# Optimization experiments

Hardware: AMD Instinct MI355X
Metric: run time of the kernel (lower is better)

Reference implementation:

```python
import jax, jax.numpy as jnp
import numpy as np

P = 16          # num_points (knots per piecewise-linear function)
LO, HI = -1.0, 1.0  # uniform knot grid range
EPS = 1e-6


def apl(x, v):
    """Adaptive piecewise-linear layer on a uniform grid.
    x: (N, I), v: (I, P, O) learnable knot values. out[n,o] = sum_i interp_i(x[n,i])."""
    I, Pk, O = v.shape
    t = (jnp.clip(x, LO, HI) - LO) / (HI - LO) * (Pk - 1)   # (N, I) in [0, P-1]
    idx = jnp.clip(jnp.floor(t), 0, Pk - 2).astype(jnp.int32)
    frac = t - idx
    ar = jnp.arange(Pk)
    # sparse interpolation weights (N, I, P): two nonzeros per (n, i)
    w = (jnp.where(ar == idx[..., None], (1.0 - frac)[..., None], 0.0)
         + jnp.where(ar == idx[..., None] + 1, frac[..., None], 0.0))
    return jnp.einsum('nip,ipo->no', w, v)


def max_abs_normalize(h):
    B, T, D = h.shape
    hn = h.reshape(B * T, D)
    hn = hn / (jnp.max(jnp.abs(hn), axis=1, keepdims=True) + EPS)
    return hn.reshape(B, T, D)


def mingru_layer(x, h0, vz, vh):
    """x: (B,T,Din), h0: (B,D). Returns normalized hidden states (B,T,D)."""
    B, T, _ = x.shape
    xf = x.reshape(B * T, -1)
    h_bar = apl(xf, vh).reshape(B, T, -1)
    z = jax.nn.sigmoid(apl(xf, vz)).reshape(B, T, -1)
    a = 1.0 - z
    b = z * h_bar
    # unstable closed-form recurrence: h[t] = A[t] * (h0 + cumsum(b/A))
    A = jnp.cumprod(a, axis=1)
    S = jnp.cumsum(b / A, axis=1)
    h = A * (h0[:, None, :] + S)
    return max_abs_normalize(h)


def setup_inputs() -> dict:
    key = jax.random.key(0)
    ks = jax.random.split(key, 8)
    B, T, Din, D, Dout = 8, 2048, 64, 64, 64
    Z_OFF = -6.0 / Din  # bias z-layer output to ~-6 so sigmoid(z) is small -> cumprod stays finite
    x = jax.random.normal(ks[0], (B, T, Din), dtype=jnp.float32)
    def vz(k, I, O):
        return 0.05 * jax.random.normal(k, (I, P, O), dtype=jnp.float32) + Z_OFF
    def vh(k, I, O):
        return 0.5 * jax.random.normal(k, (I, P, O), dtype=jnp.float32)
    return {
        'x': x,
        'vz0': vz(ks[1], Din, D), 'vh0': vh(ks[2], Din, D),
        'vz1': vz(ks[3], D, D),   'vh1': vh(ks[4], D, D),
        'vz2': vz(ks[5], D, D),   'vh2': vh(ks[6], D, D),
        'vout': 0.5 * jax.random.normal(ks[7], (D, P, Dout), dtype=jnp.float32),
    }


def reference(x, vz0, vh0, vz1, vh1, vz2, vh2, vout):
    B, T, _ = x.shape
    D = vh0.shape[-1]
    h0 = jnp.zeros((B, D), dtype=x.dtype)
    cur = mingru_layer(x, h0, vz0, vh0)
    cur = mingru_layer(cur, h0, vz1, vh1)
    cur = mingru_layer(cur, h0, vz2, vh2)
    out = apl(cur.reshape(B * T, -1), vout).reshape(B, T, -1)
    return out
```

## Files before the change

kernel.cpp:

```cpp
#include <hip/hip_runtime.h>


#define WPB 4
#define NC 64
#define CL 32

__global__ __launch_bounds__(256) void prep_dual_kernel(
    const float* __restrict__ vz, const float* __restrict__ vh,
    float4* __restrict__ tab)
{
    int idx = blockIdx.x * blockDim.x + threadIdx.x;
    if (idx >= 64 * 15 * 64) return;
    int o = idx & 63;
    int p = (idx >> 6) % 15;
    int i = idx / (15 * 64);
    int base = (i * 16 + p) * 64 + o;
    float z0 = vz[base], z1 = vz[base + 64];
    float h0 = vh[base], h1 = vh[base + 64];
    tab[idx] = make_float4(z0, z1 - z0, h0, h1 - h0);
}

__global__ __launch_bounds__(256) void prep_out_kernel(
    const float* __restrict__ v, float2* __restrict__ tab)
{
    int idx = blockIdx.x * blockDim.x + threadIdx.x;
    if (idx >= 64 * 15 * 64) return;
    int o = idx & 63;
    int p = (idx >> 6) % 15;
    int i = idx / (15 * 64);
    int base = (i * 16 + p) * 64 + o;
    float v0 = v[base], v1 = v[base + 64];
    tab[idx] = make_float2(v0, v1 - v0);
}

__global__ __launch_bounds__(256) void apl_dual_kernel(
    const float* __restrict__ in, const float4* __restrict__ tab,
    float2* __restrict__ zh, int N)
{
    int lane = threadIdx.x & 63;
    int n = blockIdx.x * WPB + (threadIdx.x >> 6);
    if (n >= N) return;

    float xv = in[(size_t)n * 64 + lane];
    float accz = 0.f, acch = 0.f;
#pragma unroll
    for (int i = 0; i < 64; ++i) {
        float xi = __shfl(xv, i, 64);
        float t = (fminf(fmaxf(xi, -1.f), 1.f) + 1.f) * 7.5f;
        int idx = (int)t;
        idx = idx > 14 ? 14 : idx;
        float fr = t - (float)idx;
        float4 e = tab[(size_t)(i * 15 + idx) * 64 + lane];
        accz += fmaf(fr, e.y, e.x);
        acch += fmaf(fr, e.w, e.z);
    }
    float z = 1.f / (1.f + expf(-accz));
    zh[(size_t)n * 64 + lane] = make_float2(z, acch);
}

__global__ __launch_bounds__(256) void apl_out_kernel(
    const float* __restrict__ in, const float2* __restrict__ tab,
    float* __restrict__ out, int N)
{
    int lane = threadIdx.x & 63;
    int n = blockIdx.x * WPB + (threadIdx.x >> 6);
    if (n >= N) return;

    float xv = in[(size_t)n * 64 + lane];
    float acc = 0.f;
#pragma unroll
    for (int i = 0; i < 64; ++i) {
        float xi = __shfl(xv, i, 64);
        float t = (fminf(fmaxf(xi, -1.f), 1.f) + 1.f) * 7.5f;
        int idx = (int)t;
        idx = idx > 14 ? 14 : idx;
        float fr = t - (float)idx;
        float2 e = tab[(size_t)(i * 15 + idx) * 64 + lane];
        acc += fmaf(fr, e.y, e.x);
    }
    out[(size_t)n * 64 + lane] = acc;
}

__global__ __launch_bounds__(256) void scan_pass1_kernel(
    const float2* __restrict__ zh, float2* __restrict__ chunkAB, int T)
{
    int lane = threadIdx.x & 63;
    int wid = blockIdx.x * (blockDim.x >> 6) + (threadIdx.x >> 6);
    int b = wid / NC, c = wid % NC;
    const float2* p = zh + ((size_t)b * T + (size_t)c * CL) * 64 + lane;

    float A = 1.f, Bc = 0.f;
    for (int k0 = 0; k0 < CL; k0 += 8) {
        float2 v[8];
#pragma unroll
        for (int k = 0; k < 8; ++k) v[k] = p[(size_t)(k0 + k) * 64];
#pragma unroll
        for (int k = 0; k < 8; ++k) {
            float a = 1.f - v[k].x;
            float bb = v[k].x * v[k].y;
            A *= a;
            Bc = fmaf(a, Bc, bb);
        }
    }
    chunkAB[(size_t)wid * 64 + lane] = make_float2(A, Bc);
}

__global__ __launch_bounds__(64) void scan_fixup_kernel(
    const float2* __restrict__ chunkAB, float* __restrict__ hinit)
{
    int b = blockIdx.x;
    int d = threadIdx.x;
    const float2* p = chunkAB + (size_t)b * NC * 64 + d;
    float* o = hinit + (size_t)b * NC * 64 + d;

    float h = 0.f;
    for (int c0 = 0; c0 < NC; c0 += 8) {
        float2 ab[8];
#pragma unroll
        for (int k = 0; k < 8; ++k) ab[k] = p[(size_t)(c0 + k) * 64];
#pragma unroll
        for (int k = 0; k < 8; ++k) {
            o[(size_t)(c0 + k) * 64] = h;
            h = fmaf(ab[k].x, h, ab[k].y);
        }
    }
}

__global__ __launch_bounds__(256) void scan_pass2_kernel(
    const float2* __restrict__ zh, const float* __restrict__ hinit,
    float* __restrict__ out, int T)
{
    int lane = threadIdx.x & 63;
    int wid = blockIdx.x * (blockDim.x >> 6) + (threadIdx.x >> 6);
    int b = wid / NC, c = wid % NC;
    const float2* p = zh + ((size_t)b * T + (size_t)c * CL) * 64 + lane;
    float* o = out + ((size_t)b * T + (size_t)c * CL) * 64 + lane;

    float h = hinit[(size_t)wid * 64 + lane];
    for (int k0 = 0; k0 < CL; k0 += 8) {
        float2 v[8];
        float hs[8];
#pragma unroll
        for (int k = 0; k < 8; ++k) v[k] = p[(size_t)(k0 + k) * 64];
#pragma unroll
        for (int k = 0; k < 8; ++k) {
            h = fmaf(v[k].x, v[k].y - h, h);
            hs[k] = h;
        }
#pragma unroll
        for (int k = 0; k < 8; ++k) {
            float m = fabsf(hs[k]);
            m = fmaxf(m, __shfl_xor(m, 32, 64));
            m = fmaxf(m, __shfl_xor(m, 16, 64));
            m = fmaxf(m, __shfl_xor(m, 8, 64));
            m = fmaxf(m, __shfl_xor(m, 4, 64));
            m = fmaxf(m, __shfl_xor(m, 2, 64));
            m = fmaxf(m, __shfl_xor(m, 1, 64));
            o[(size_t)(k0 + k) * 64] = hs[k] / (m + 1e-6f);
        }
    }
}

extern "C" void kernel_launch(void* const* d_in, const int* in_sizes, int n_in,
                              void* d_out, int out_size, void* d_ws, size_t ws_size,
                              hipStream_t stream) {
    const float* x    = (const float*)d_in[0];
    const float* vz0  = (const float*)d_in[1];
    const float* vh0  = (const float*)d_in[2];
    const float* vz1  = (const float*)d_in[3];
    const float* vh1  = (const float*)d_in[4];
    const float* vz2  = (const float*)d_in[5];
    const float* vh2  = (const float*)d_in[6];
    const float* vout = (const float*)d_in[7];

    const int N = in_sizes[0] / 64;
    const int T = NC * CL;
    const int B = N / T;

    char* ws = (char*)d_ws;
    const size_t TAB_ELEMS = (size_t)64 * 15 * 64;
    float2* zh      = (float2*)ws;
    float*  cur     = (float*)(ws + 8388608);
    float4* tab0    = (float4*)(ws + 12582912);
    float4* tab1    = (float4*)(ws + 13565952);
    float4* tab2    = (float4*)(ws + 14548992);
    float2* tab_out = (float2*)(ws + 15532032);
    float2* chunkAB = (float2*)(ws + 16023552);
    float*  hinit   = (float*)(ws + 16285696);

    dim3 pblk(256), pgrd((TAB_ELEMS + 255) / 256);
    prep_dual_kernel<<<pgrd, pblk, 0, stream>>>(vz0, vh0, tab0);
    prep_dual_kernel<<<pgrd, pblk, 0, stream>>>(vz1, vh1, tab1);
    prep_dual_kernel<<<pgrd, pblk, 0, stream>>>(vz2, vh2, tab2);
    prep_out_kernel<<<pgrd, pblk, 0, stream>>>(vout, tab_out);

    dim3 ablk(256), agrd((N + WPB - 1) / WPB);
    dim3 sblk(256), sgrd(B * NC / 4);

    const float4* tabs[3] = {tab0, tab1, tab2};
    const float* layer_in = x;
    for (int l = 0; l < 3; ++l) {
        apl_dual_kernel<<<agrd, ablk, 0, stream>>>(layer_in, tabs[l], zh, N);
        scan_pass1_kernel<<<sgrd, sblk, 0, stream>>>(zh, chunkAB, T);
        scan_fixup_kernel<<<B, 64, 0, stream>>>(chunkAB, hinit);
        scan_pass2_kernel<<<sgrd, sblk, 0, stream>>>(zh, hinit, cur, T);
        layer_in = cur;
    }
    apl_out_kernel<<<agrd, ablk, 0, stream>>>(cur, tab_out, (float*)d_out, N);
}
```

Before: 195.9 us.

## Tile APL kernels over 64 rows with LDS-staged, double-buffered knot tables

```diff
diff --git a/kernel.cpp b/kernel.cpp
--- a/kernel.cpp
+++ b/kernel.cpp
@@ -1,7 +1,6 @@
 #include <hip/hip_runtime.h>
 
 
-#define WPB 4
 #define NC 64
 #define CL 32
 
@@ -33,52 +32,151 @@
     tab[idx] = make_float2(v0, v1 - v0);
 }
 
-__global__ __launch_bounds__(256) void apl_dual_kernel(
+__global__ __launch_bounds__(256) void apl_dual_lds_kernel(
     const float* __restrict__ in, const float4* __restrict__ tab,
-    float2* __restrict__ zh, int N)
-{
-    int lane = threadIdx.x & 63;
-    int n = blockIdx.x * WPB + (threadIdx.x >> 6);
-    if (n >= N) return;
-
-    float xv = in[(size_t)n * 64 + lane];
-    float accz = 0.f, acch = 0.f;
-#pragma unroll
+    float2* __restrict__ zh)
+{
+    __shared__ float tS[64][64];
+    __shared__ float4 tabs[2][960];
+
+    const int tid = threadIdx.x;
+    const int lane = tid & 63;
+    const int w = tid >> 6;
+    const size_t base = (size_t)blockIdx.x * 64;
+
+    for (int r = tid; r < 1024; r += 256) {
+        float4 xv = ((const float4*)in)[base * 16 + r];
+        int s = r >> 4;
+        int i0 = (r & 15) << 2;
+        tS[i0 + 0][s] = fminf(fmaxf(xv.x, -1.f), 1.f) * 7.5f + 7.5f;
+        tS[i0 + 1][s] = fminf(fmaxf(xv.y, -1.f), 1.f) * 7.5f + 7.5f;
+        tS[i0 + 2][s] = fminf(fmaxf(xv.z, -1.f), 1.f) * 7.5f + 7.5f;
+        tS[i0 + 3][s] = fminf(fmaxf(xv.w, -1.f), 1.f) * 7.5f + 7.5f;
+    }
+    {
+        tabs[0][tid]       = tab[tid];
+        tabs[0][tid + 256] = tab[tid + 256];
+        tabs[0][tid + 512] = tab[tid + 512];
+        if (tid < 192) tabs[0][tid + 768] = tab[tid + 768];
+    }
+    __syncthreads();
+
+    float accz[16], acch[16];
+#pragma unroll
+    for (int k = 0; k < 16; ++k) { accz[k] = 0.f; acch[k] = 0.f; }
+
     for (int i = 0; i < 64; ++i) {
-        float xi = __shfl(xv, i, 64);
-        float t = (fminf(fmaxf(xi, -1.f), 1.f) + 1.f) * 7.5f;
-        int idx = (int)t;
-        idx = idx > 14 ? 14 : idx;
-        float fr = t - (float)idx;
-        float4 e = tab[(size_t)(i * 15 + idx) * 64 + lane];
-        accz += fmaf(fr, e.y, e.x);
-        acch += fmaf(fr, e.w, e.z);
-    }
-    float z = 1.f / (1.f + expf(-accz));
-    zh[(size_t)n * 64 + lane] = make_float2(z, acch);
-}
-
-__global__ __launch_bounds__(256) void apl_out_kernel(
+        const int buf = i & 1;
+        float4 p0, p1, p2, p3;
+        if (i < 63) {
+            const float4* src = tab + (size_t)(i + 1) * 960;
+            p0 = src[tid]; p1 = src[tid + 256]; p2 = src[tid + 512];
+            if (tid < 192) p3 = src[tid + 768];
+        }
+        const float4* trow = (const float4*)(&tS[i][w * 16]);
+#pragma unroll
+        for (int q = 0; q < 4; ++q) {
+            float4 tq = trow[q];
+            float tv0 = tq.x, tv1 = tq.y, tv2 = tq.z, tv3 = tq.w;
+            float tarr[4] = {tv0, tv1, tv2, tv3};
+#pragma unroll
+            for (int j = 0; j < 4; ++j) {
+                float t = tarr[j];
+                int idx = (int)t; idx = idx > 14 ? 14 : idx;
+                float fr = t - (float)idx;
+                float4 e = tabs[buf][idx * 64 + lane];
+                accz[q * 4 + j] += fmaf(fr, e.y, e.x);
+                acch[q * 4 + j] += fmaf(fr, e.w, e.z);
+            }
+        }
+        __syncthreads();
+        if (i < 63) {
+            tabs[buf ^ 1][tid]       = p0;
+            tabs[buf ^ 1][tid + 256] = p1;
+            tabs[buf ^ 1][tid + 512] = p2;
+            if (tid < 192) tabs[buf ^ 1][tid + 768] = p3;
+        }
+        __syncthreads();
+    }
+
+#pragma unroll
+    for (int k = 0; k < 16; ++k) {
+        int s = w * 16 + k;
+        float z = 1.f / (1.f + expf(-accz[k]));
+        zh[(base + s) * 64 + lane] = make_float2(z, acch[k]);
+    }
+}
+
+__global__ __launch_bounds__(256) void apl_out_lds_kernel(
     const float* __restrict__ in, const float2* __restrict__ tab,
-    float* __restrict__ out, int N)
-{
-    int lane = threadIdx.x & 63;
-    int n = blockIdx.x * WPB + (threadIdx.x >> 6);
-    if (n >= N) return;
-
-    float xv = in[(size_t)n * 64 + lane];
-    float acc = 0.f;
-#pragma unroll
+    float* __restrict__ out)
+{
+    __shared__ float tS[64][64];
+    __shared__ float2 tabs[2][960];
+
+    const int tid = threadIdx.x;
+    const int lane = tid & 63;
+    const int w = tid >> 6;
+    const size_t base = (size_t)blockIdx.x * 64;
+
+    for (int r = tid; r < 1024; r += 256) {
+        float4 xv = ((const float4*)in)[base * 16 + r];
+        int s = r >> 4;
+        int i0 = (r & 15) << 2;
+        tS[i0 + 0][s] = fminf(fmaxf(xv.x, -1.f), 1.f) * 7.5f + 7.5f;
+        tS[i0 + 1][s] = fminf(fmaxf(xv.y, -1.f), 1.f) * 7.5f + 7.5f;
+        tS[i0 + 2][s] = fminf(fmaxf(xv.z, -1.f), 1.f) * 7.5f + 7.5f;
+        tS[i0 + 3][s] = fminf(fmaxf(xv.w, -1.f), 1.f) * 7.5f + 7.5f;
+    }
+    {
+        tabs[0][tid]       = tab[tid];
+        tabs[0][tid + 256] = tab[tid + 256];
+        tabs[0][tid + 512] = tab[tid + 512];
+        if (tid < 192) tabs[0][tid + 768] = tab[tid + 768];
+    }
+    __syncthreads();
+
+    float acc[16];
+#pragma unroll
+    for (int k = 0; k < 16; ++k) acc[k] = 0.f;
+
     for (int i = 0; i < 64; ++i) {
-        float xi = __shfl(xv, i, 64);
-        float t = (fminf(fmaxf(xi, -1.f), 1.f) + 1.f) * 7.5f;
-        int idx = (int)t;
-        idx = idx > 14 ? 14 : idx;
-        float fr = t - (float)idx;
-        float2 e = tab[(size_t)(i * 15 + idx) * 64 + lane];
-        acc += fmaf(fr, e.y, e.x);
-    }
-    out[(size_t)n * 64 + lane] = acc;
+        const int buf = i & 1;
+        float2 p0, p1, p2, p3;
+        if (i < 63) {
+            const float2* src = tab + (size_t)(i + 1) * 960;
+            p0 = src[tid]; p1 = src[tid + 256]; p2 = src[tid + 512];
+            if (tid < 192) p3 = src[tid + 768];
+        }
+        const float4* trow = (const float4*)(&tS[i][w * 16]);
+#pragma unroll
+        for (int q = 0; q < 4; ++q) {
+            float4 tq = trow[q];
+            float tarr[4] = {tq.x, tq.y, tq.z, tq.w};
+#pragma unroll
+            for (int j = 0; j < 4; ++j) {
+                float t = tarr[j];
+                int idx = (int)t; idx = idx > 14 ? 14 : idx;
+                float fr = t - (float)idx;
+                float2 e = tabs[buf][idx * 64 + lane];
+                acc[q * 4 + j] += fmaf(fr, e.y, e.x);
+            }
+        }
+        __syncthreads();
+        if (i < 63) {
+            tabs[buf ^ 1][tid]       = p0;
+            tabs[buf ^ 1][tid + 256] = p1;
+            tabs[buf ^ 1][tid + 512] = p2;
+            if (tid < 192) tabs[buf ^ 1][tid + 768] = p3;
+        }
+        __syncthreads();
+    }
+
+#pragma unroll
+    for (int k = 0; k < 16; ++k) {
+        int s = w * 16 + k;
+        out[(base + s) * 64 + lane] = acc[k];
+    }
 }
 
 __global__ __launch_bounds__(256) void scan_pass1_kernel(
@@ -176,6 +274,7 @@
     const int N = in_sizes[0] / 64;
     const int T = NC * CL;
     const int B = N / T;
+    const int NBLK = N / 64;
 
     char* ws = (char*)d_ws;
     const size_t TAB_ELEMS = (size_t)64 * 15 * 64;
@@ -194,17 +293,16 @@
     prep_dual_kernel<<<pgrd, pblk, 0, stream>>>(vz2, vh2, tab2);
     prep_out_kernel<<<pgrd, pblk, 0, stream>>>(vout, tab_out);
 
-    dim3 ablk(256), agrd((N + WPB - 1) / WPB);
     dim3 sblk(256), sgrd(B * NC / 4);
 
     const float4* tabs[3] = {tab0, tab1, tab2};
     const float* layer_in = x;
     for (int l = 0; l < 3; ++l) {
-        apl_dual_kernel<<<agrd, ablk, 0, stream>>>(layer_in, tabs[l], zh, N);
+        apl_dual_lds_kernel<<<NBLK, 256, 0, stream>>>(layer_in, tabs[l], zh);
         scan_pass1_kernel<<<sgrd, sblk, 0, stream>>>(zh, chunkAB, T);
         scan_fixup_kernel<<<B, 64, 0, stream>>>(chunkAB, hinit);
         scan_pass2_kernel<<<sgrd, sblk, 0, stream>>>(zh, hinit, cur, T);
         layer_in = cur;
     }
-    apl_out_kernel<<<agrd, ablk, 0, stream>>>(cur, tab_out, (float*)d_out, N);
-}
+    apl_out_lds_kernel<<<NBLK, 256, 0, stream>>>(cur, tab_out, (float*)d_out);
+}
```

Measured after the change: 245.3 us. 1.25x slower.
